# Kernel optimization log

Hardware: AMD Instinct MI355X
Metric: run time of the kernel (lower is better)

## Reference

```python
import jax, jax.numpy as jnp
import numpy as np

D_MODEL = 1024
EXPAND = 2
HEADDIM = 64
D_STATE = 64
CHUNK = 64
D_INNER = EXPAND * D_MODEL          # 2048
NHEADS = D_INNER // HEADDIM         # 32
D_MLP = int(2.5 * D_MODEL)          # 2560
BATCH = 2
SEQLEN = 4096
PROJ = 2 * D_INNER + 2 * NHEADS * D_STATE + NHEADS + NHEADS * (D_STATE // 2)


def rmsnorm(x, w, eps=1e-5):
    return x * jax.lax.rsqrt(jnp.mean(x * x, axis=-1, keepdims=True) + eps) * w


def apply_rope(x, angles):
    x1 = x[..., 0::2]
    x2 = x[..., 1::2]
    c = jnp.cos(angles)
    s = jnp.sin(angles)
    ev = c * x1 - s * x2
    od = s * x1 + c * x2
    return jnp.stack([ev, od], axis=-1).reshape(x.shape)


def segsum(x):
    # x: (b,h,c,l) -> (b,h,c,l,l); [i,j] = sum_{j<k<=i} x_k (no -inf mask, as in source)
    T = x.shape[-1]
    xx = jnp.broadcast_to(x[..., :, None], x.shape + (T,))
    mask = jnp.tril(jnp.ones((T, T), dtype=bool), -1)
    xx = jnp.where(mask, xx, 0.0)
    return jnp.cumsum(xx, axis=-2)


def ssd(x, A, B, C, chunk):
    # x: (b,s,h,p), A: (b,s,h), B/C: (b,s,h,n); s % chunk == 0
    b, s, h, p = x.shape
    n = B.shape[-1]
    c = s // chunk
    x_c = x.reshape(b, c, chunk, h, p).transpose(0, 1, 3, 2, 4)  # (b,c,h,l,p)
    B_c = B.reshape(b, c, chunk, h, n).transpose(0, 1, 3, 2, 4)  # (b,c,h,l,n)
    C_c = C.reshape(b, c, chunk, h, n).transpose(0, 1, 3, 2, 4)
    A_c = A.reshape(b, c, chunk, h).transpose(0, 1, 3, 2)        # (b,c,h,l)
    A_cum = jnp.cumsum(A_c, axis=-1)
    L = jnp.exp(segsum(A_c.transpose(0, 2, 1, 3))).transpose(0, 2, 1, 3, 4)  # (b,c,h,l,l)
    Bx = jnp.einsum('bchln,bchlp->bchpn', B_c, x_c)
    Y_diag = jnp.einsum('bchln,bchls,bchpn->bchlp', C_c, L, Bx)
    decay_states = jnp.exp(A_cum[..., -1:] - A_cum)
    states = jnp.einsum('bchln,bchl,bchlp->bchpn', B_c, decay_states, x_c)  # (b,c,h,p,n)
    decay_chunk = jnp.exp(A_cum[..., -1])  # (b,c,h)
    h0 = jnp.zeros_like(states[:, 0])

    def step(carry, inp):
        dec, st = inp  # dec: (b,h), st: (b,h,p,n)
        carry = carry * dec[:, :, None, None] + st
        return carry, carry

    _, hs = jax.lax.scan(step, h0, (decay_chunk.transpose(1, 0, 2),
                                    states.transpose(1, 0, 2, 3, 4)))
    final_states = hs.transpose(1, 0, 2, 3, 4)  # (b,c,h,p,n)
    Y_off = jnp.einsum('bchln,bchpn,bchl->bchlp', C_c, final_states, jnp.exp(A_cum))
    Y = (Y_diag + Y_off).transpose(0, 1, 3, 2, 4).reshape(b, s, h * p)
    return Y


def setup_inputs() -> dict:
    key = jax.random.key(0)
    ks = jax.random.split(key, 12)
    sc = 0.02
    return {
        'x': jax.random.normal(ks[0], (BATCH, SEQLEN, D_MODEL), jnp.float32),
        'norm1_w': jnp.ones((D_MODEL,), jnp.float32),
        'norm2_w': jnp.ones((D_MODEL,), jnp.float32),
        'W_in': sc * jax.random.normal(ks[1], (D_MODEL, PROJ), jnp.float32),
        'W_out': sc * jax.random.normal(ks[2], (D_INNER, D_MODEL), jnp.float32),
        'A_log': jax.random.uniform(ks[3], (NHEADS,), jnp.float32, -4.0, -1.0),
        'D_param': jnp.ones((NHEADS,), jnp.float32),
        'dt_bias': jax.random.uniform(ks[4], (NHEADS,), jnp.float32, 0.001, 0.1),
        'B_bias': jnp.ones((1, NHEADS, D_STATE), jnp.float32),
        'C_bias': jnp.ones((1, NHEADS, D_STATE), jnp.float32),
        'Bn_w': jnp.ones((D_STATE,), jnp.float32),
        'Cn_w': jnp.ones((D_STATE,), jnp.float32),
        'Wg': sc * jax.random.normal(ks[5], (D_MODEL, D_MLP), jnp.float32),
        'Wu': sc * jax.random.normal(ks[6], (D_MODEL, D_MLP), jnp.float32),
        'Wd': sc * jax.random.normal(ks[7], (D_MLP, D_MODEL), jnp.float32),
    }


def reference(x, norm1_w, norm2_w, W_in, W_out, A_log, D_param, dt_bias,
              B_bias, C_bias, Bn_w, Cn_w, Wg, Wu, Wd):
    b, s, _ = x.shape
    h = rmsnorm(x, norm1_w)
    proj = h @ W_in
    i = 0
    z = proj[..., i:i + D_INNER]; i += D_INNER
    x_ssm = proj[..., i:i + D_INNER]; i += D_INNER
    B = proj[..., i:i + NHEADS * D_STATE].reshape(b, s, NHEADS, D_STATE); i += NHEADS * D_STATE
    C = proj[..., i:i + NHEADS * D_STATE].reshape(b, s, NHEADS, D_STATE); i += NHEADS * D_STATE
    dt = proj[..., i:i + NHEADS]; i += NHEADS
    theta = proj[..., i:].reshape(b, s, NHEADS, D_STATE // 2)
    dt = jax.nn.softplus(dt + dt_bias)                 # (b,s,h)
    A = -jnp.exp(A_log) * dt
    alpha = jnp.exp(A)
    gamma = (alpha - 1.0) / (A + 1e-6) * 0.5 + 1.0
    B = rmsnorm(B, Bn_w) + B_bias
    C = rmsnorm(C, Cn_w) + C_bias
    cum_theta = jnp.cumsum(dt[..., None] * theta, axis=1)
    B = apply_rope(B, cum_theta)
    C = apply_rope(C, cum_theta)
    x_ssm = x_ssm.reshape(b, s, NHEADS, HEADDIM)
    y = ssd(x_ssm * gamma[..., None], A, B, C, CHUNK)
    skip = jnp.broadcast_to((D_param * x_ssm.sum(-1))[..., None], x_ssm.shape)
    y = y + skip.reshape(b, s, -1)
    y = y * (z * jax.nn.sigmoid(z))
    y = y @ W_out
    x = x + y
    h2 = rmsnorm(x, norm2_w)
    g = h2 @ Wg
    x = x + ((g * jax.nn.sigmoid(g)) * (h2 @ Wu)) @ Wd
    return x
```

## Files before the change

### kernel.cpp

```cpp
#include <hip/hip_runtime.h>
#include <cstdint>
#include <cmath>


typedef __bf16 bf16;
typedef __bf16 bf16x2 __attribute__((ext_vector_type(2)));
typedef __bf16 bf16x4 __attribute__((ext_vector_type(4)));
typedef __bf16 bf16x8 __attribute__((ext_vector_type(8)));
typedef float fx4 __attribute__((ext_vector_type(4)));

#define DEV __device__ __forceinline__

#define OFF_PROJ    0ull
#define OFF_HHI     134217728ull
#define OFF_HLO     150994944ull
#define OFF_WTIN    167772160ull
#define OFF_WTHI    184549376ull
#define OFF_WTLO    186908672ull
#define OFF_PROJT   189267968ull
#define OFF_BX      189267968ull
#define OFF_STATES  222822400ull
#define OFF_WTOUT   222822400ull
#define OFF_WTGU    227016704ull
#define OFF_WTD     237502464ull
#define OFF_ABUF    256376832ull
#define OFF_XSUM    257425408ull
#define OFF_ROWSUM  258473984ull
#define OFF_EXPA    260571136ull
#define OFF_DCHUNK  262668288ull
#define OFF_GAMMA   262684672ull
#define WS_NEEDED   263733248ull

#define OFF_GU      0ull
#define OFF_MBF     83886080ull

DEV void async_copy16(void* lds, const void* gptr) {
  __builtin_amdgcn_global_load_lds(
      (const __attribute__((address_space(1))) unsigned int*)(gptr),
      (__attribute__((address_space(3))) unsigned int*)(lds),
      16, 0, 0);
}

DEV float warp_sum64(float v) {
  #pragma unroll
  for (int o = 32; o; o >>= 1) v += __shfl_xor(v, o);
  return v;
}

DEV float red16(float v) {
  v += __shfl_xor(v, 1); v += __shfl_xor(v, 2);
  v += __shfl_xor(v, 4); v += __shfl_xor(v, 8);
  return v;
}

DEV float softplus_f(float x) { return x > 20.f ? x : log1pf(expf(x)); }
DEV float sigmoid_f(float x) { return 1.f / (1.f + expf(-x)); }

__global__ __launch_bounds__(256) void transpose_cast(
    const float* __restrict__ src, int ld, int col0,
    bf16* __restrict__ dst, int R, int C)
{
  __shared__ float tile[32][33];
  const int c0 = blockIdx.x * 32, r0 = blockIdx.y * 32;
  const int tx = threadIdx.x & 31, ty = threadIdx.x >> 5;
  #pragma unroll
  for (int ii = 0; ii < 4; ++ii) {
    int i = ty + ii * 8;
    int c = c0 + tx;
    tile[i][tx] = (c < C) ? src[(size_t)(r0 + i) * ld + col0 + c] : 0.f;
  }
  __syncthreads();
  #pragma unroll
  for (int ii = 0; ii < 4; ++ii) {
    int i = ty + ii * 8;
    dst[(size_t)(c0 + i) * R + r0 + tx] = (bf16)tile[tx][i];
  }
}

__global__ __launch_bounds__(256) void transpose_cast_hilo(
    const float* __restrict__ src, int ld, int col0,
    bf16* __restrict__ dhi, bf16* __restrict__ dlo, int R, int C)
{
  __shared__ float tile[32][33];
  const int c0 = blockIdx.x * 32, r0 = blockIdx.y * 32;
  const int tx = threadIdx.x & 31, ty = threadIdx.x >> 5;
  #pragma unroll
  for (int ii = 0; ii < 4; ++ii) {
    int i = ty + ii * 8;
    int c = c0 + tx;
    tile[i][tx] = (c < C) ? src[(size_t)(r0 + i) * ld + col0 + c] : 0.f;
  }
  __syncthreads();
  #pragma unroll
  for (int ii = 0; ii < 4; ++ii) {
    int i = ty + ii * 8;
    float v = tile[tx][i];
    bf16 hi = (bf16)v;
    size_t o = (size_t)(c0 + i) * R + r0 + tx;
    dhi[o] = hi;
    dlo[o] = (bf16)(v - (float)hi);
  }
}

__global__ __launch_bounds__(256) void rmsnorm_kernel(
    const float* __restrict__ x, const float* __restrict__ w,
    bf16* __restrict__ hi, bf16* __restrict__ lo)
{
  __shared__ float red[4];
  const size_t row = blockIdx.x;
  const int tid = threadIdx.x;
  float4 v = ((const float4*)(x + row * 1024))[tid];
  float ss = v.x * v.x + v.y * v.y + v.z * v.z + v.w * v.w;
  ss = warp_sum64(ss);
  if ((tid & 63) == 0) red[tid >> 6] = ss;
  __syncthreads();
  float tot = red[0] + red[1] + red[2] + red[3];
  float s = rsqrtf(tot * (1.f / 1024.f) + 1e-5f);
  float4 wv = ((const float4*)w)[tid];
  float h0 = v.x * s * wv.x, h1 = v.y * s * wv.y, h2 = v.z * s * wv.z, h3 = v.w * s * wv.w;
  bf16x4 hv = { (bf16)h0, (bf16)h1, (bf16)h2, (bf16)h3 };
  *(bf16x4*)(hi + row * 1024 + tid * 4) = hv;
  if (lo) {
    bf16x4 lv = { (bf16)(h0 - (float)hv[0]), (bf16)(h1 - (float)hv[1]),
                  (bf16)(h2 - (float)hv[2]), (bf16)(h3 - (float)hv[3]) };
    *(bf16x4*)(lo + row * 1024 + tid * 4) = lv;
  }
}

template <int MODE>
__global__ __launch_bounds__(256) void gemm_bt(
    const bf16* A, const bf16* B, void* Cout, const float* resid,
    int K, int lda, int ldc)
{
  __shared__ bf16 As[128 * 64];
  __shared__ bf16 Bs[128 * 64];
  const int tid = threadIdx.x, wid = tid >> 6, lane = tid & 63;
  const int m0 = blockIdx.y * 128, n0 = blockIdx.x * 128;
  const int wm = (wid & 1) * 64, wn = (wid >> 1) * 64;
  fx4 acc[4][4];
  #pragma unroll
  for (int i = 0; i < 4; ++i)
    #pragma unroll
    for (int j = 0; j < 4; ++j) { fx4 z = {0.f, 0.f, 0.f, 0.f}; acc[i][j] = z; }

  const int srow = wid * 32 + (lane >> 3);
  const int slot = lane & 7;

  for (int k0 = 0; k0 < K; k0 += 64) {
    __syncthreads();
    #pragma unroll
    for (int i = 0; i < 4; ++i) {
      int m = srow + i * 8;
      int cA = ((slot ^ (m & 7)) * 8);
      async_copy16(&As[wid * 2048 + i * 512], A + (size_t)(m0 + m) * lda + k0 + cA);
    }
    #pragma unroll
    for (int i = 0; i < 4; ++i) {
      int n = srow + i * 8;
      int cB = ((slot ^ (n & 7)) * 8);
      async_copy16(&Bs[wid * 2048 + i * 512], B + (size_t)(n0 + n) * K + k0 + cB);
    }
    __syncthreads();
    #pragma unroll
    for (int kk = 0; kk < 2; ++kk) {
      bf16x8 af[4], bfr[4];
      #pragma unroll
      for (int i = 0; i < 4; ++i) {
        int mm = wm + i * 16 + (lane & 15);
        int sA = (kk * 4 + (lane >> 4)) ^ (mm & 7);
        af[i] = *(const bf16x8*)&As[mm * 64 + sA * 8];
        int nn = wn + i * 16 + (lane & 15);
        int sB = (kk * 4 + (lane >> 4)) ^ (nn & 7);
        bfr[i] = *(const bf16x8*)&Bs[nn * 64 + sB * 8];
      }
      #pragma unroll
      for (int i = 0; i < 4; ++i)
        #pragma unroll
        for (int j = 0; j < 4; ++j)
          acc[i][j] = __builtin_amdgcn_mfma_f32_16x16x32_bf16(af[i], bfr[j], acc[i][j], 0, 0, 0);
    }
  }
  const int r0 = (lane >> 4) * 4, cc = lane & 15;
  #pragma unroll
  for (int i = 0; i < 4; ++i) {
    #pragma unroll
    for (int j = 0; j < 4; ++j) {
      #pragma unroll
      for (int r = 0; r < 4; ++r) {
        int m = m0 + wm + i * 16 + r0 + r;
        int n = n0 + wn + j * 16 + cc;
        size_t off = (size_t)m * ldc + n;
        float v = acc[i][j][r];
        if (MODE == 1) ((bf16*)Cout)[off] = (bf16)v;
        else ((float*)Cout)[off] = v + resid[off];
      }
    }
  }
}

__global__ __launch_bounds__(256) void gemm_tail(
    const bf16* Ahi, const bf16* Alo, const bf16* Whi, const bf16* Wlo,
    float* Cout)
{
  __shared__ bf16 Ah[128 * 64], Al[128 * 64], Bh[128 * 64], Bl[128 * 64];
  const int tid = threadIdx.x, wid = tid >> 6, lane = tid & 63;
  const int m0 = blockIdx.y * 128, n0 = blockIdx.x * 128;
  const int wm = (wid & 1) * 64, wn = (wid >> 1) * 64;
  fx4 acc[4][4];
  #pragma unroll
  for (int i = 0; i < 4; ++i)
    #pragma unroll
    for (int j = 0; j < 4; ++j) { fx4 z = {0.f, 0.f, 0.f, 0.f}; acc[i][j] = z; }

  const int srow = wid * 32 + (lane >> 3);
  const int slot = lane & 7;

  for (int k0 = 0; k0 < 1024; k0 += 64) {
    __syncthreads();
    #pragma unroll
    for (int i = 0; i < 4; ++i) {
      int m = srow + i * 8;
      int cA = ((slot ^ (m & 7)) * 8);
      size_t ao = (size_t)(m0 + m) * 1024 + k0 + cA;
      async_copy16(&Ah[wid * 2048 + i * 512], Ahi + ao);
      async_copy16(&Al[wid * 2048 + i * 512], Alo + ao);
      int n = srow + i * 8;
      int cB = ((slot ^ (n & 7)) * 8);
      size_t bo = (size_t)(n0 + n) * 1024 + k0 + cB;
      async_copy16(&Bh[wid * 2048 + i * 512], Whi + bo);
      async_copy16(&Bl[wid * 2048 + i * 512], Wlo + bo);
    }
    __syncthreads();
    #pragma unroll
    for (int kk = 0; kk < 2; ++kk) {
      bf16x8 ah[4], al[4], bh[4], bl[4];
      #pragma unroll
      for (int i = 0; i < 4; ++i) {
        int mm = wm + i * 16 + (lane & 15);
        int sA = (kk * 4 + (lane >> 4)) ^ (mm & 7);
        ah[i] = *(const bf16x8*)&Ah[mm * 64 + sA * 8];
        al[i] = *(const bf16x8*)&Al[mm * 64 + sA * 8];
        int nn = wn + i * 16 + (lane & 15);
        int sB = (kk * 4 + (lane >> 4)) ^ (nn & 7);
        bh[i] = *(const bf16x8*)&Bh[nn * 64 + sB * 8];
        bl[i] = *(const bf16x8*)&Bl[nn * 64 + sB * 8];
      }
      #pragma unroll
      for (int i = 0; i < 4; ++i)
        #pragma unroll
        for (int j = 0; j < 4; ++j) {
          acc[i][j] = __builtin_amdgcn_mfma_f32_16x16x32_bf16(ah[i], bh[j], acc[i][j], 0, 0, 0);
          acc[i][j] = __builtin_amdgcn_mfma_f32_16x16x32_bf16(ah[i], bl[j], acc[i][j], 0, 0, 0);
          acc[i][j] = __builtin_amdgcn_mfma_f32_16x16x32_bf16(al[i], bh[j], acc[i][j], 0, 0, 0);
        }
    }
  }
  const int r0 = (lane >> 4) * 4, cc = lane & 15;
  #pragma unroll
  for (int i = 0; i < 4; ++i)
    #pragma unroll
    for (int j = 0; j < 4; ++j)
      #pragma unroll
      for (int r = 0; r < 4; ++r) {
        int m = m0 + wm + i * 16 + r0 + r;
        int n = n0 + wn + j * 16 + cc;
        Cout[(size_t)m * 1152 + n] = acc[i][j][r];
      }
}

__global__ __launch_bounds__(256) void dt_kernel(
    float* projT, const float* __restrict__ A_log, const float* __restrict__ dt_bias,
    float* __restrict__ a_buf, float* __restrict__ gamma_buf)
{
  const int idx = blockIdx.x * 256 + threadIdx.x;
  const int t = idx >> 5, h = idx & 31;
  float dtr = projT[(size_t)t * 1152 + h] + dt_bias[h];
  float dt = softplus_f(dtr);
  float a = -expf(A_log[h]) * dt;
  float alpha = expf(a);
  float gamma = (alpha - 1.f) / (a + 1e-6f) * 0.5f + 1.f;
  projT[(size_t)t * 1152 + h] = dt;
  a_buf[idx] = a;
  gamma_buf[idx] = gamma;
}

__global__ __launch_bounds__(512, 2) void gemm_proj256(
    const bf16* __restrict__ A, const bf16* __restrict__ B, bf16* __restrict__ Cout,
    const float* __restrict__ gamma_buf, float* __restrict__ xsum,
    const float* __restrict__ Bn_w, const float* __restrict__ Cn_w,
    const float* __restrict__ B_bias, const float* __restrict__ C_bias)
{
  __shared__ bf16 lds[65536];
  const int tid = threadIdx.x, wid = tid >> 6, lane = tid & 63;
  const int bid = blockIdx.x;
  const int swz = (bid & 7) * 128 + (bid >> 3);
  const int by = swz >> 5, bx = swz & 31;
  const int m0 = by * 256, n0 = bx * 256;
  const int wr = wid >> 2, wc = wid & 3;
  const int fl = lane & 15, fq = lane >> 4;
  const int rloc = wid * 8 + (lane >> 3);
  const int colSwz = ((lane & 7) ^ (lane >> 3)) * 8;

  fx4 acc[8][4];
  #pragma unroll
  for (int i = 0; i < 8; ++i)
    #pragma unroll
    for (int j = 0; j < 4; ++j) { fx4 z = {0.f, 0.f, 0.f, 0.f}; acc[i][j] = z; }

  const bf16* gA = A + (size_t)(m0 + rloc) * 1024 + colSwz;
  const bf16* gB = B + (size_t)(n0 + rloc) * 1024 + colSwz;

  auto STAGE = [&](int u, int h) {
    const bf16* s = (h < 2) ? gB : gA;
    s += (size_t)(h & 1) * 128 * 1024 + u * 64;
    bf16* d = &lds[((u & 1) * 4 + h) * 8192 + wid * 512];
    async_copy16(d, s);
    async_copy16(d + 4096, s + 64 * 1024);
  };

  STAGE(0, 0); STAGE(0, 1); STAGE(0, 2); STAGE(0, 3);
  STAGE(1, 0); STAGE(1, 1);
  asm volatile("s_waitcnt vmcnt(4)" ::: "memory");
  __builtin_amdgcn_s_barrier();

  const int NT = 16;
  bf16x8 bfrag[4][2];
  for (int t = 0; t < NT; ++t) {
    const int Bb = (t & 1) * 32768;
    const int Ab = Bb + 16384;
    #pragma unroll
    for (int p = 0; p < 4; ++p) {
      bf16x8 af[2][2];
      if (p == 0) {
        #pragma unroll
        for (int j = 0; j < 4; ++j) {
          int nn = wc * 64 + j * 16 + fl;
          #pragma unroll
          for (int kk = 0; kk < 2; ++kk) {
            int q = (kk * 4 + fq) ^ (nn & 7);
            bfrag[j][kk] = *(const bf16x8*)&lds[Bb + nn * 64 + q * 8];
          }
        }
      }
      #pragma unroll
      for (int ii = 0; ii < 2; ++ii) {
        int mm = wr * 128 + (p * 2 + ii) * 16 + fl;
        #pragma unroll
        for (int kk = 0; kk < 2; ++kk) {
          int q = (kk * 4 + fq) ^ (mm & 7);
          af[ii][kk] = *(const bf16x8*)&lds[Ab + mm * 64 + q * 8];
        }
      }
      {
        int H = 4 * t + 6 + p;
        if (H < 4 * NT) STAGE(H >> 2, H & 3);
      }
      if (p == 3) asm volatile("s_waitcnt vmcnt(4)" ::: "memory");
      __builtin_amdgcn_s_barrier();
      asm volatile("s_waitcnt lgkmcnt(0)" ::: "memory");
      __builtin_amdgcn_sched_barrier(0);
      __builtin_amdgcn_s_setprio(1);
      #pragma unroll
      for (int ii = 0; ii < 2; ++ii)
        #pragma unroll
        for (int j = 0; j < 4; ++j)
          #pragma unroll
          for (int kk = 0; kk < 2; ++kk)
            acc[p * 2 + ii][j] = __builtin_amdgcn_mfma_f32_16x16x32_bf16(
                af[ii][kk], bfrag[j][kk], acc[p * 2 + ii][j], 0, 0, 0);
      __builtin_amdgcn_s_setprio(0);
      __builtin_amdgcn_s_barrier();
    }
  }

  const int reg = bx >> 3;
  const int hh = ((n0 + wc * 64) & 2047) >> 6;
  const int mwb = m0 + wr * 128;
  const int nwb = n0 + wc * 64;
  if (reg == 0) {
    #pragma unroll
    for (int i = 0; i < 8; ++i)
      #pragma unroll
      for (int j = 0; j < 4; ++j)
        #pragma unroll
        for (int r = 0; r < 4; ++r) {
          int m = mwb + i * 16 + fq * 4 + r;
          int n = nwb + j * 16 + fl;
          Cout[(size_t)m * 8192 + n] = (bf16)acc[i][j][r];
        }
  } else if (reg == 1) {
    #pragma unroll
    for (int i = 0; i < 8; ++i)
      #pragma unroll
      for (int r = 0; r < 4; ++r) {
        float s = acc[i][0][r] + acc[i][1][r] + acc[i][2][r] + acc[i][3][r];
        s = red16(s);
        int m = mwb + i * 16 + fq * 4 + r;
        if (fl == 0) xsum[(size_t)m * 32 + hh] = s;
        float g = gamma_buf[(size_t)m * 32 + hh];
        #pragma unroll
        for (int j = 0; j < 4; ++j) {
          int n = nwb + j * 16 + fl;
          Cout[(size_t)m * 8192 + n] = (bf16)(acc[i][j][r] * g);
        }
      }
  } else {
    const float* w = (reg == 2) ? Bn_w : Cn_w;
    const float* bias = (reg == 2) ? B_bias : C_bias;
    #pragma unroll
    for (int i = 0; i < 8; ++i)
      #pragma unroll
      for (int r = 0; r < 4; ++r) {
        float ss = acc[i][0][r] * acc[i][0][r] + acc[i][1][r] * acc[i][1][r]
                 + acc[i][2][r] * acc[i][2][r] + acc[i][3][r] * acc[i][3][r];
        ss = red16(ss);
        float sc = rsqrtf(ss * (1.f / 64.f) + 1e-5f);
        int m = mwb + i * 16 + fq * 4 + r;
        #pragma unroll
        for (int j = 0; j < 4; ++j) {
          int c = j * 16 + fl;
          Cout[(size_t)m * 8192 + nwb + c] =
              (bf16)(acc[i][j][r] * sc * w[c] + bias[hh * 64 + c]);
        }
      }
  }
}

__global__ __launch_bounds__(256) void chunk_sum_kernel(
    const float* __restrict__ projT, float* __restrict__ S)
{
  __shared__ float lds[8 * 288];
  const int blk = blockIdx.x;
  const int hq = blockIdx.y;
  const size_t row0 = (size_t)blk * 64;
  const int tid = threadIdx.x;
  float s = 0.f;
  #pragma unroll 1
  for (int batch = 0; batch < 8; ++batch) {
    __syncthreads();
    const float* src = projT + (row0 + batch * 8) * 1152;
    #pragma unroll
    for (int i = 0; i < 9; ++i) {
      int idx = i * 256 + tid;
      int r = idx / 288, col = idx - r * 288;
      int gcol = (col < 32) ? col : (32 + hq * 256 + (col - 32));
      lds[idx] = src[r * 1152 + gcol];
    }
    __syncthreads();
    int hl = tid >> 5, d = tid & 31;
    #pragma unroll
    for (int r = 0; r < 8; ++r)
      s += lds[r * 288 + hq * 8 + hl] * lds[r * 288 + 32 + hl * 32 + d];
  }
  S[(size_t)blk * 1024 + hq * 256 + tid] = s;
}

__global__ __launch_bounds__(256) void rope_kernel(
    bf16* proj, const float* __restrict__ projT, const float* __restrict__ S)
{
  __shared__ float angs[64 * 33], angc[64 * 33];
  const int blk = blockIdx.x;
  const int b = blk >> 11, c = (blk >> 5) & 63, h = blk & 31;
  const size_t t0 = (size_t)b * 4096 + c * 64;
  const int w = threadIdx.x >> 6, lane = threadIdx.x & 63;
  const float* tr = projT + (t0 + lane) * 1152;
  float dtv = tr[h];
  const float* thp = tr + 32 + h * 32 + w * 8;
  float4 th0 = *(const float4*)thp;
  float4 th1 = *(const float4*)(thp + 4);
  const float* Sp = S + (size_t)(b * 64 + lane) * 1024 + h * 32 + w * 8;
  float4 S0 = *(const float4*)Sp;
  float4 S1 = *(const float4*)(Sp + 4);
  float th[8] = { th0.x, th0.y, th0.z, th0.w, th1.x, th1.y, th1.z, th1.w };
  float Sv[8] = { S0.x, S0.y, S0.z, S0.w, S1.x, S1.y, S1.z, S1.w };
  #pragma unroll 1
  for (int j = 0; j < 8; ++j) {
    int d = w * 8 + j;
    float sv = (lane < c) ? Sv[j] : 0.f;
    float off = warp_sum64(sv);
    float v = dtv * th[j];
    #pragma unroll
    for (int o = 1; o < 64; o <<= 1) { float u = __shfl_up(v, o); if (lane >= o) v += u; }
    float ang = off + v;
    float sn, cs;
    sincosf(ang, &sn, &cs);
    angs[lane * 33 + d] = sn;
    angc[lane * 33 + d] = cs;
  }
  __syncthreads();
  const int tt = threadIdx.x >> 2, q = threadIdx.x & 3;
  const size_t base = (t0 + tt) * 8192 + 4096 + h * 64 + q * 16;
  #pragma unroll
  for (int m = 0; m < 2; ++m) {
    bf16* p = proj + base + m * 2048;
    bf16x8 v0 = *(const bf16x8*)(p);
    bf16x8 v1 = *(const bf16x8*)(p + 8);
    bf16x8 r0, r1;
    #pragma unroll
    for (int pp = 0; pp < 4; ++pp) {
      int d = q * 8 + pp;
      float e1 = (float)v0[2 * pp], e2 = (float)v0[2 * pp + 1];
      float sn = angs[tt * 33 + d], cs = angc[tt * 33 + d];
      r0[2 * pp]     = (bf16)(cs * e1 - sn * e2);
      r0[2 * pp + 1] = (bf16)(sn * e1 + cs * e2);
    }
    #pragma unroll
    for (int pp = 0; pp < 4; ++pp) {
      int d = q * 8 + 4 + pp;
      float e1 = (float)v1[2 * pp], e2 = (float)v1[2 * pp + 1];
      float sn = angs[tt * 33 + d], cs = angc[tt * 33 + d];
      r1[2 * pp]     = (bf16)(cs * e1 - sn * e2);
      r1[2 * pp + 1] = (bf16)(sn * e1 + cs * e2);
    }
    *(bf16x8*)(p) = r0;
    *(bf16x8*)(p + 8) = r1;
  }
}

__global__ __launch_bounds__(256) void ssd1_kernel(
    const bf16* __restrict__ proj, const float* __restrict__ a_buf,
    bf16* __restrict__ Bx, bf16* __restrict__ states,
    float* __restrict__ rowsum, float* __restrict__ expac, float* __restrict__ dchunk)
{
  __shared__ bf16 Xs[64 * 72], Bs[64 * 72];
  __shared__ float acum[64], dsv[64];
  const int blk = blockIdx.x;
  const int h = blk & 31;
  const size_t bs0 = ((size_t)(blk >> 5)) * 64;
  const int tid = threadIdx.x;
  const int l = tid >> 2, p0 = (tid & 3) * 16;
  {
    const bf16* xrow = proj + (bs0 + l) * 8192 + 2048 + h * 64 + p0;
    *(bf16x8*)&Xs[l * 72 + p0]     = ((const bf16x8*)xrow)[0];
    *(bf16x8*)&Xs[l * 72 + p0 + 8] = ((const bf16x8*)xrow)[1];
    const bf16* brow = proj + (bs0 + l) * 8192 + 4096 + h * 64 + p0;
    *(bf16x8*)&Bs[l * 72 + p0]     = ((const bf16x8*)brow)[0];
    *(bf16x8*)&Bs[l * 72 + p0 + 8] = ((const bf16x8*)brow)[1];
  }
  if (tid < 64) {
    float v = a_buf[(bs0 + tid) * 32 + h];
    #pragma unroll
    for (int o = 1; o < 64; o <<= 1) { float u = __shfl_up(v, o); if (tid >= o) v += u; }
    acum[tid] = v;
    float a63 = __shfl(v, 63);
    dsv[tid] = expf(a63 - v);
    expac[(size_t)blk * 64 + tid] = expf(v);
    if (tid == 63) dchunk[blk] = expf(v);
  }
  __syncthreads();
  {
    float al = acum[l];
    float rs = 0.f;
    for (int s = tid & 3; s <= l; s += 4) rs += expf(al - acum[s]);
    rs += __shfl_xor(rs, 1);
    rs += __shfl_xor(rs, 2);
    if ((tid & 3) == 0) rowsum[(size_t)blk * 64 + l] = rs + (float)(63 - l);
  }
  const int wv = tid >> 6, lane = tid & 63;
  const int mi = lane & 15, kq = lane >> 4;
  const int m0 = wv * 16;
  fx4 accB[4], accS[4];
  #pragma unroll
  for (int j4 = 0; j4 < 4; ++j4) { fx4 z = {0.f,0.f,0.f,0.f}; accB[j4] = z; accS[j4] = z; }
  #pragma unroll
  for (int kk = 0; kk < 2; ++kk) {
    const int lb = kk * 32 + kq * 8;
    bf16x8 aX, aXd;
    #pragma unroll
    for (int j = 0; j < 8; ++j) {
      bf16 xv = Xs[(lb + j) * 72 + m0 + mi];
      aX[j] = xv;
      aXd[j] = (bf16)((float)xv * dsv[lb + j]);
    }
    #pragma unroll
    for (int j4 = 0; j4 < 4; ++j4) {
      bf16x8 bB;
      #pragma unroll
      for (int j = 0; j < 8; ++j) bB[j] = Bs[(lb + j) * 72 + j4 * 16 + mi];
      accB[j4] = __builtin_amdgcn_mfma_f32_16x16x32_bf16(aX, bB, accB[j4], 0, 0, 0);
      accS[j4] = __builtin_amdgcn_mfma_f32_16x16x32_bf16(aXd, bB, accS[j4], 0, 0, 0);
    }
  }
  const size_t obase = (size_t)blk * 4096;
  #pragma unroll
  for (int j4 = 0; j4 < 4; ++j4) {
    #pragma unroll
    for (int r = 0; r < 4; ++r) {
      int p = m0 + kq * 4 + r;
      int n = j4 * 16 + mi;
      Bx[obase + p * 64 + n] = (bf16)accB[j4][r];
      states[obase + p * 64 + n] = (bf16)accS[j4][r];
    }
  }
}

__global__ __launch_bounds__(128) void ssd2_kernel(
    bf16* __restrict__ states, const float* __restrict__ dchunk)
{
  const int blk = blockIdx.x;
  const int b = blk >> 9, rest = blk & 511;
  const int h = rest >> 4, q = rest & 15;
  const int e0 = q * 256 + threadIdx.x * 2;
  float fs0 = 0.f, fs1 = 0.f;
  #pragma unroll 2
  for (int c = 0; c < 64; ++c) {
    size_t idx = ((size_t)(b * 2048 + c * 32 + h) * 4096) + e0;
    float dec = dchunk[b * 2048 + c * 32 + h];
    bf16x2 st = *(const bf16x2*)(states + idx);
    fs0 = fs0 * dec + (float)st[0];
    fs1 = fs1 * dec + (float)st[1];
    bf16x2 o = { (bf16)fs0, (bf16)fs1 };
    *(bf16x2*)(states + idx) = o;
  }
}

__global__ __launch_bounds__(256) void ssd3_kernel(
    bf16* proj, const bf16* __restrict__ Bx, const bf16* __restrict__ FS,
    const float* __restrict__ rowsum, const float* __restrict__ expac,
    const float* __restrict__ xsum, const float* __restrict__ D_param)
{
  __shared__ bf16 Cs[64 * 72], BxS[64 * 72], FSs[64 * 72];
  __shared__ float rs_s[64], ea_s[64], sk_s[64];
  const int blk = blockIdx.x;
  const int h = blk & 31;
  const size_t bs0 = ((size_t)(blk >> 5)) * 64;
  const int tid = threadIdx.x;
  const int l = tid >> 2, q0 = (tid & 3) * 16;
  {
    const bf16* crow = proj + (bs0 + l) * 8192 + 6144 + h * 64 + q0;
    *(bf16x8*)&Cs[l * 72 + q0]     = ((const bf16x8*)crow)[0];
    *(bf16x8*)&Cs[l * 72 + q0 + 8] = ((const bf16x8*)crow)[1];
    size_t mb = (size_t)blk * 4096 + l * 64 + q0;
    *(bf16x8*)&BxS[l * 72 + q0]     = ((const bf16x8*)(Bx + mb))[0];
    *(bf16x8*)&BxS[l * 72 + q0 + 8] = ((const bf16x8*)(Bx + mb))[1];
    *(bf16x8*)&FSs[l * 72 + q0]     = ((const bf16x8*)(FS + mb))[0];
    *(bf16x8*)&FSs[l * 72 + q0 + 8] = ((const bf16x8*)(FS + mb))[1];
  }
  if (tid < 64) {
    rs_s[tid] = rowsum[(size_t)blk * 64 + tid];
    ea_s[tid] = expac[(size_t)blk * 64 + tid];
    sk_s[tid] = D_param[h] * xsum[(bs0 + tid) * 32 + h];
  }
  __syncthreads();
  const int wv = tid >> 6, lane = tid & 63;
  const int mi = lane & 15, kq = lane >> 4;
  const int m0 = wv * 16;
  fx4 acc1[4], acc2[4];
  #pragma unroll
  for (int j4 = 0; j4 < 4; ++j4) { fx4 z = {0.f,0.f,0.f,0.f}; acc1[j4] = z; acc2[j4] = z; }
  #pragma unroll
  for (int kk = 0; kk < 2; ++kk) {
    bf16x8 aC = *(const bf16x8*)&Cs[(m0 + mi) * 72 + kk * 32 + kq * 8];
    #pragma unroll
    for (int j4 = 0; j4 < 4; ++j4) {
      bf16x8 bx = *(const bf16x8*)&BxS[(j4 * 16 + mi) * 72 + kk * 32 + kq * 8];
      bf16x8 fs = *(const bf16x8*)&FSs[(j4 * 16 + mi) * 72 + kk * 32 + kq * 8];
      acc1[j4] = __builtin_amdgcn_mfma_f32_16x16x32_bf16(aC, bx, acc1[j4], 0, 0, 0);
      acc2[j4] = __builtin_amdgcn_mfma_f32_16x16x32_bf16(aC, fs, acc2[j4], 0, 0, 0);
    }
  }
  #pragma unroll
  for (int j4 = 0; j4 < 4; ++j4) {
    #pragma unroll
    for (int r = 0; r < 4; ++r) {
      int li = m0 + kq * 4 + r;
      int p = j4 * 16 + mi;
      float y = rs_s[li] * acc1[j4][r] + ea_s[li] * acc2[j4][r] + sk_s[li];
      size_t zoff = (bs0 + li) * 8192 + h * 64 + p;
      float z = (float)proj[zoff];
      proj[zoff + 2048] = (bf16)(y * z * sigmoid_f(z));
    }
  }
}

__global__ __launch_bounds__(256) void silu_mul_kernel(
    const bf16* __restrict__ gu, bf16* __restrict__ m)
{
  const size_t row = blockIdx.y;
  const int col2 = blockIdx.x * 256 + threadIdx.x;
  const size_t gi = row * 5120 + col2 * 2;
  bf16x2 g = *(const bf16x2*)(gu + gi);
  bf16x2 u = *(const bf16x2*)(gu + gi + 2560);
  float g0 = (float)g[0], g1 = (float)g[1];
  float m0 = g0 * sigmoid_f(g0) * (float)u[0];
  float m1 = g1 * sigmoid_f(g1) * (float)u[1];
  bf16x2 mv = { (bf16)m0, (bf16)m1 };
  *(bf16x2*)(m + row * 2560 + col2 * 2) = mv;
}

extern "C" void kernel_launch(void* const* d_in, const int* in_sizes, int n_in,
                              void* d_out, int out_size, void* d_ws, size_t ws_size,
                              hipStream_t stream) {
  (void)in_sizes; (void)n_in; (void)out_size;
  if (ws_size < WS_NEEDED) return;
  const float* x       = (const float*)d_in[0];
  const float* n1w     = (const float*)d_in[1];
  const float* n2w     = (const float*)d_in[2];
  const float* W_in    = (const float*)d_in[3];
  const float* W_out   = (const float*)d_in[4];
  const float* A_log   = (const float*)d_in[5];
  const float* D_param = (const float*)d_in[6];
  const float* dt_bias = (const float*)d_in[7];
  const float* B_bias  = (const float*)d_in[8];
  const float* C_bias  = (const float*)d_in[9];
  const float* Bn_w    = (const float*)d_in[10];
  const float* Cn_w    = (const float*)d_in[11];
  const float* Wg      = (const float*)d_in[12];
  const float* Wu      = (const float*)d_in[13];
  const float* Wd      = (const float*)d_in[14];
  float* out = (float*)d_out;
  char* ws = (char*)d_ws;

  bf16*  proj   = (bf16*)(ws + OFF_PROJ);
  float* projT  = (float*)(ws + OFF_PROJT);
  bf16*  h_hi   = (bf16*)(ws + OFF_HHI);
  bf16*  h_lo   = (bf16*)(ws + OFF_HLO);
  bf16*  Wt_in  = (bf16*)(ws + OFF_WTIN);
  bf16*  Wt_hi  = (bf16*)(ws + OFF_WTHI);
  bf16*  Wt_lo  = (bf16*)(ws + OFF_WTLO);
  bf16*  Wt_out = (bf16*)(ws + OFF_WTOUT);
  bf16*  Wt_gu  = (bf16*)(ws + OFF_WTGU);
  bf16*  Wt_d   = (bf16*)(ws + OFF_WTD);
  bf16*  Bx     = (bf16*)(ws + OFF_BX);
  bf16*  states = (bf16*)(ws + OFF_STATES);
  float* a_buf  = (float*)(ws + OFF_ABUF);
  float* xsum_  = (float*)(ws + OFF_XSUM);
  float* rowsum = (float*)(ws + OFF_ROWSUM);
  float* expac  = (float*)(ws + OFF_EXPA);
  float* dchunk = (float*)(ws + OFF_DCHUNK);
  float* gamma_ = (float*)(ws + OFF_GAMMA);
  float* Ssum   = (float*)(ws + OFF_HLO);
  bf16*  ybf    = proj + 2048;
  bf16*  gubf   = (bf16*)(ws + OFF_GU);
  bf16*  mbf    = (bf16*)(ws + OFF_MBF);
  bf16*  h2bf   = h_hi;
  float* x2     = out;

  transpose_cast<<<dim3(256, 32), 256, 0, stream>>>(W_in, 9248, 0, Wt_in, 1024, 8192);
  transpose_cast_hilo<<<dim3(36, 32), 256, 0, stream>>>(W_in, 9248, 8192, Wt_hi, Wt_lo, 1024, 1056);

  rmsnorm_kernel<<<8192, 256, 0, stream>>>(x, n1w, h_hi, h_lo);

  gemm_tail<<<dim3(9, 64), 256, 0, stream>>>(h_hi, h_lo, Wt_hi, Wt_lo, projT);
  dt_kernel<<<1024, 256, 0, stream>>>(projT, A_log, dt_bias, a_buf, gamma_);
  gemm_proj256<<<dim3(1024), 512, 0, stream>>>(h_hi, Wt_in, proj, gamma_, xsum_,
                                               Bn_w, Cn_w, B_bias, C_bias);

  chunk_sum_kernel<<<dim3(128, 4), 256, 0, stream>>>(projT, Ssum);
  rope_kernel<<<4096, 256, 0, stream>>>(proj, projT, Ssum);

  ssd1_kernel<<<4096, 256, 0, stream>>>(proj, a_buf, Bx, states, rowsum, expac, dchunk);
  ssd2_kernel<<<1024, 128, 0, stream>>>(states, dchunk);
  ssd3_kernel<<<4096, 256, 0, stream>>>(proj, Bx, states, rowsum, expac, xsum_, D_param);

  transpose_cast<<<dim3(32, 64), 256, 0, stream>>>(W_out, 1024, 0, Wt_out, 2048, 1024);
  transpose_cast<<<dim3(80, 32), 256, 0, stream>>>(Wg, 2560, 0, Wt_gu, 1024, 2560);
  transpose_cast<<<dim3(80, 32), 256, 0, stream>>>(Wu, 2560, 0, Wt_gu + (size_t)2560 * 1024, 1024, 2560);
  transpose_cast<<<dim3(32, 80), 256, 0, stream>>>(Wd, 1024, 0, Wt_d, 2560, 1024);

  gemm_bt<2><<<dim3(8, 64), 256, 0, stream>>>(ybf, Wt_out, x2, x, 2048, 8192, 1024);

  rmsnorm_kernel<<<8192, 256, 0, stream>>>(x2, n2w, h2bf, nullptr);
  gemm_bt<1><<<dim3(40, 64), 256, 0, stream>>>(h2bf, Wt_gu, gubf, nullptr, 1024, 1024, 5120);
  silu_mul_kernel<<<dim3(5, 8192), 256, 0, stream>>>(gubf, mbf);
  gemm_bt<2><<<dim3(8, 64), 256, 0, stream>>>(mbf, Wt_d, out, x2, 2560, 2560, 1024);
}
```

Measured before the change: 812.9 us.

## Use 256x256-tile pipelined bf16 GEMM for the MLP gate/up projection

Replaces the generic gemm_bt call for the fused gate/up projection (8192x1024 by 5120) with a new 256x256-tile kernel of 512 threads. It uses double-buffered async global-to-LDS copies, an XOR-swizzled LDS layout, a block-index swizzle for L2 locality, and interleaved MFMA phases with priority hints. The aim is more data reuse per tile and better overlap of loads with compute. The cost is a large LDS footprint and high register use, which limit occupancy, plus a grid of 640 blocks that may leave the tail unbalanced.

```diff
diff --git a/kernel.cpp b/kernel.cpp
--- a/kernel.cpp
+++ b/kernel.cpp
@@ -424,6 +424,109 @@
         }
       }
   }
+}
+
+__global__ __launch_bounds__(512, 2) void gemm256_bf16(
+    const bf16* __restrict__ A, const bf16* __restrict__ B, bf16* __restrict__ Cout,
+    int NT, int lda, int ldc, int nbx)
+{
+  __shared__ bf16 lds[65536];
+  const int tid = threadIdx.x, wid = tid >> 6, lane = tid & 63;
+  const int cpx = gridDim.x >> 3;
+  const int bid = blockIdx.x;
+  const int swz = (bid & 7) * cpx + (bid >> 3);
+  const int by = swz / nbx, bx = swz - by * nbx;
+  const int m0 = by * 256, n0 = bx * 256;
+  const int wr = wid >> 2, wc = wid & 3;
+  const int fl = lane & 15, fq = lane >> 4;
+  const int rloc = wid * 8 + (lane >> 3);
+  const int colSwz = ((lane & 7) ^ (lane >> 3)) * 8;
+  const int K = NT * 64;
+
+  fx4 acc[8][4];
+  #pragma unroll
+  for (int i = 0; i < 8; ++i)
+    #pragma unroll
+    for (int j = 0; j < 4; ++j) { fx4 z = {0.f, 0.f, 0.f, 0.f}; acc[i][j] = z; }
+
+  const bf16* gA = A + (size_t)(m0 + rloc) * lda + colSwz;
+  const bf16* gB = B + (size_t)(n0 + rloc) * K + colSwz;
+
+  auto STAGE = [&](int u, int h) {
+    const bf16* s = (h < 2) ? gB : gA;
+    const size_t str = (h < 2) ? (size_t)K : (size_t)lda;
+    s += (size_t)(h & 1) * 128 * str + u * 64;
+    bf16* d = &lds[((u & 1) * 4 + h) * 8192 + wid * 512];
+    async_copy16(d, s);
+    async_copy16(d + 4096, s + 64 * str);
+  };
+
+  STAGE(0, 0); STAGE(0, 1); STAGE(0, 2); STAGE(0, 3);
+  STAGE(1, 0); STAGE(1, 1);
+  asm volatile("s_waitcnt vmcnt(4)" ::: "memory");
+  __builtin_amdgcn_s_barrier();
+
+  bf16x8 bfrag[4][2];
+  for (int t = 0; t < NT; ++t) {
+    const int Bb = (t & 1) * 32768;
+    const int Ab = Bb + 16384;
+    #pragma unroll
+    for (int p = 0; p < 4; ++p) {
+      bf16x8 af[2][2];
+      if (p == 0) {
+        #pragma unroll
+        for (int j = 0; j < 4; ++j) {
+          int nn = wc * 64 + j * 16 + fl;
+          #pragma unroll
+          for (int kk = 0; kk < 2; ++kk) {
+            int q = (kk * 4 + fq) ^ (nn & 7);
+            bfrag[j][kk] = *(const bf16x8*)&lds[Bb + nn * 64 + q * 8];
+          }
+        }
+      }
+      #pragma unroll
+      for (int ii = 0; ii < 2; ++ii) {
+        int mm = wr * 128 + (p * 2 + ii) * 16 + fl;
+        #pragma unroll
+        for (int kk = 0; kk < 2; ++kk) {
+          int q = (kk * 4 + fq) ^ (mm & 7);
+          af[ii][kk] = *(const bf16x8*)&lds[Ab + mm * 64 + q * 8];
+        }
+      }
+      {
+        int H = 4 * t + 6 + p;
+        if (H < 4 * NT) STAGE(H >> 2, H & 3);
+      }
+      if (p == 3) asm volatile("s_waitcnt vmcnt(4)" ::: "memory");
+      __builtin_amdgcn_s_barrier();
+      asm volatile("s_waitcnt lgkmcnt(0)" ::: "memory");
+      __builtin_amdgcn_sched_barrier(0);
+      __builtin_amdgcn_s_setprio(1);
+      #pragma unroll
+      for (int ii = 0; ii < 2; ++ii)
+        #pragma unroll
+        for (int j = 0; j < 4; ++j)
+          #pragma unroll
+          for (int kk = 0; kk < 2; ++kk)
+            acc[p * 2 + ii][j] = __builtin_amdgcn_mfma_f32_16x16x32_bf16(
+                af[ii][kk], bfrag[j][kk], acc[p * 2 + ii][j], 0, 0, 0);
+      __builtin_amdgcn_s_setprio(0);
+      __builtin_amdgcn_s_barrier();
+    }
+  }
+
+  const int mwb = m0 + wr * 128;
+  const int nwb = n0 + wc * 64;
+  #pragma unroll
+  for (int i = 0; i < 8; ++i)
+    #pragma unroll
+    for (int j = 0; j < 4; ++j)
+      #pragma unroll
+      for (int r = 0; r < 4; ++r) {
+        int m = mwb + i * 16 + fq * 4 + r;
+        int n = nwb + j * 16 + fl;
+        Cout[(size_t)m * ldc + n] = (bf16)acc[i][j][r];
+      }
 }
 
 __global__ __launch_bounds__(256) void chunk_sum_kernel(
@@ -761,7 +864,7 @@
   gemm_bt<2><<<dim3(8, 64), 256, 0, stream>>>(ybf, Wt_out, x2, x, 2048, 8192, 1024);
 
   rmsnorm_kernel<<<8192, 256, 0, stream>>>(x2, n2w, h2bf, nullptr);
-  gemm_bt<1><<<dim3(40, 64), 256, 0, stream>>>(h2bf, Wt_gu, gubf, nullptr, 1024, 1024, 5120);
+  gemm256_bf16<<<dim3(640), 512, 0, stream>>>(h2bf, Wt_gu, gubf, 16, 1024, 5120, 20);
   silu_mul_kernel<<<dim3(5, 8192), 256, 0, stream>>>(gubf, mbf);
   gemm_bt<2><<<dim3(8, 64), 256, 0, stream>>>(mbf, Wt_d, out, x2, 2560, 2560, 1024);
 }
```

New measurement: 831.7 us. 2.3% more time.

## Replace output and MLP GEMMs with pipelined 128x256 double-buffered kernel

Applied to the files above, without the earlier changes.

Replaces the simple 128x128 single-stage GEMM used for the out-projection and MLP with a 512-thread 128x256 tile kernel. It double-buffers LDS with staggered async copies interleaved among the MFMA phases, uses grouped block-index swizzling for L2 locality, and raises wave priority around MFMA bursts. The goal is to hide global-load latency and raise MFMA utilisation. In exchange it uses more LDS (96KB per block) and more barriers, and it assumes dimensions divide the tile sizes.

```diff
diff --git a/kernel.cpp b/kernel.cpp
--- a/kernel.cpp
+++ b/kernel.cpp
@@ -127,77 +127,6 @@
   }
 }
 
-template <int MODE>
-__global__ __launch_bounds__(256) void gemm_bt(
-    const bf16* A, const bf16* B, void* Cout, const float* resid,
-    int K, int lda, int ldc)
-{
-  __shared__ bf16 As[128 * 64];
-  __shared__ bf16 Bs[128 * 64];
-  const int tid = threadIdx.x, wid = tid >> 6, lane = tid & 63;
-  const int m0 = blockIdx.y * 128, n0 = blockIdx.x * 128;
-  const int wm = (wid & 1) * 64, wn = (wid >> 1) * 64;
-  fx4 acc[4][4];
-  #pragma unroll
-  for (int i = 0; i < 4; ++i)
-    #pragma unroll
-    for (int j = 0; j < 4; ++j) { fx4 z = {0.f, 0.f, 0.f, 0.f}; acc[i][j] = z; }
-
-  const int srow = wid * 32 + (lane >> 3);
-  const int slot = lane & 7;
-
-  for (int k0 = 0; k0 < K; k0 += 64) {
-    __syncthreads();
-    #pragma unroll
-    for (int i = 0; i < 4; ++i) {
-      int m = srow + i * 8;
-      int cA = ((slot ^ (m & 7)) * 8);
-      async_copy16(&As[wid * 2048 + i * 512], A + (size_t)(m0 + m) * lda + k0 + cA);
-    }
-    #pragma unroll
-    for (int i = 0; i < 4; ++i) {
-      int n = srow + i * 8;
-      int cB = ((slot ^ (n & 7)) * 8);
-      async_copy16(&Bs[wid * 2048 + i * 512], B + (size_t)(n0 + n) * K + k0 + cB);
-    }
-    __syncthreads();
-    #pragma unroll
-    for (int kk = 0; kk < 2; ++kk) {
-      bf16x8 af[4], bfr[4];
-      #pragma unroll
-      for (int i = 0; i < 4; ++i) {
-        int mm = wm + i * 16 + (lane & 15);
-        int sA = (kk * 4 + (lane >> 4)) ^ (mm & 7);
-        af[i] = *(const bf16x8*)&As[mm * 64 + sA * 8];
-        int nn = wn + i * 16 + (lane & 15);
-        int sB = (kk * 4 + (lane >> 4)) ^ (nn & 7);
-        bfr[i] = *(const bf16x8*)&Bs[nn * 64 + sB * 8];
-      }
-      #pragma unroll
-      for (int i = 0; i < 4; ++i)
-        #pragma unroll
-        for (int j = 0; j < 4; ++j)
-          acc[i][j] = __builtin_amdgcn_mfma_f32_16x16x32_bf16(af[i], bfr[j], acc[i][j], 0, 0, 0);
-    }
-  }
-  const int r0 = (lane >> 4) * 4, cc = lane & 15;
-  #pragma unroll
-  for (int i = 0; i < 4; ++i) {
-    #pragma unroll
-    for (int j = 0; j < 4; ++j) {
-      #pragma unroll
-      for (int r = 0; r < 4; ++r) {
-        int m = m0 + wm + i * 16 + r0 + r;
-        int n = n0 + wn + j * 16 + cc;
-        size_t off = (size_t)m * ldc + n;
-        float v = acc[i][j][r];
-        if (MODE == 1) ((bf16*)Cout)[off] = (bf16)v;
-        else ((float*)Cout)[off] = v + resid[off];
-      }
-    }
-  }
-}
-
 __global__ __launch_bounds__(256) void gemm_tail(
     const bf16* Ahi, const bf16* Alo, const bf16* Whi, const bf16* Wlo,
     float* Cout)
@@ -424,6 +353,110 @@
         }
       }
   }
+}
+
+template <int MODE>
+__global__ __launch_bounds__(512, 2) void gemm128x256(
+    const bf16* __restrict__ A, const bf16* __restrict__ B, void* __restrict__ Cout,
+    const float* __restrict__ resid, int NT, int lda, int ldc, int nbx)
+{
+  __shared__ bf16 lds[49152];
+  const int tid = threadIdx.x, wid = tid >> 6, lane = tid & 63;
+  const int cpx = gridDim.x >> 3;
+  const int bid = blockIdx.x;
+  const int swz = (bid & 7) * cpx + (bid >> 3);
+  const int by = swz / nbx, bx = swz - by * nbx;
+  const int m0 = by * 128, n0 = bx * 256;
+  const int wr = wid >> 2, wc = wid & 3;
+  const int fl = lane & 15, fq = lane >> 4;
+  const int rloc = wid * 8 + (lane >> 3);
+  const int colSwz = ((lane & 7) ^ (lane >> 3)) * 8;
+  const int K = NT * 64;
+
+  fx4 acc[4][4];
+  #pragma unroll
+  for (int i = 0; i < 4; ++i)
+    #pragma unroll
+    for (int j = 0; j < 4; ++j) { fx4 z = {0.f, 0.f, 0.f, 0.f}; acc[i][j] = z; }
+
+  const bf16* gA = A + (size_t)(m0 + rloc) * lda + colSwz;
+  const bf16* gB = B + (size_t)(n0 + rloc) * K + colSwz;
+
+  auto STAGE = [&](int u, int h) {
+    const bf16* s;
+    size_t str;
+    if (h < 2) { s = gB + (size_t)h * 128 * K; str = (size_t)K; }
+    else       { s = gA;                       str = (size_t)lda; }
+    s += u * 64;
+    bf16* d = &lds[((u & 1) * 3 + h) * 8192 + wid * 512];
+    async_copy16(d, s);
+    async_copy16(d + 4096, s + 64 * str);
+  };
+
+  STAGE(0, 0); STAGE(0, 1); STAGE(0, 2);
+  STAGE(1, 0); STAGE(1, 1);
+  asm volatile("s_waitcnt vmcnt(4)" ::: "memory");
+  __builtin_amdgcn_s_barrier();
+
+  bf16x8 bfrag[4][2];
+  for (int t = 0; t < NT; ++t) {
+    const int base = (t & 1) * 24576;
+    #pragma unroll
+    for (int p = 0; p < 4; ++p) {
+      bf16x8 af[2];
+      if (p == 0) {
+        #pragma unroll
+        for (int j = 0; j < 4; ++j) {
+          int nn = wc * 64 + j * 16 + fl;
+          #pragma unroll
+          for (int kk = 0; kk < 2; ++kk) {
+            int q = (kk * 4 + fq) ^ (nn & 7);
+            bfrag[j][kk] = *(const bf16x8*)&lds[base + (nn >> 7) * 8192 + (nn & 127) * 64 + q * 8];
+          }
+        }
+      }
+      {
+        int mm = wr * 64 + p * 16 + fl;
+        #pragma unroll
+        for (int kk = 0; kk < 2; ++kk) {
+          int q = (kk * 4 + fq) ^ (mm & 7);
+          af[kk] = *(const bf16x8*)&lds[base + 2 * 8192 + mm * 64 + q * 8];
+        }
+      }
+      if (p == 0)      { if (t + 1 < NT) STAGE(t + 1, 2); }
+      else if (p == 1) { if (t + 2 < NT) STAGE(t + 2, 0); }
+      else if (p == 2) { if (t + 2 < NT) STAGE(t + 2, 1); }
+      if (p == 3) asm volatile("s_waitcnt vmcnt(4)" ::: "memory");
+      __builtin_amdgcn_s_barrier();
+      asm volatile("s_waitcnt lgkmcnt(0)" ::: "memory");
+      __builtin_amdgcn_sched_barrier(0);
+      __builtin_amdgcn_s_setprio(1);
+      #pragma unroll
+      for (int j = 0; j < 4; ++j)
+        #pragma unroll
+        for (int kk = 0; kk < 2; ++kk)
+          acc[p][j] = __builtin_amdgcn_mfma_f32_16x16x32_bf16(
+              af[kk], bfrag[j][kk], acc[p][j], 0, 0, 0);
+      __builtin_amdgcn_s_setprio(0);
+      __builtin_amdgcn_s_barrier();
+    }
+  }
+
+  const int mwb = m0 + wr * 64;
+  const int nwb = n0 + wc * 64;
+  #pragma unroll
+  for (int i = 0; i < 4; ++i)
+    #pragma unroll
+    for (int j = 0; j < 4; ++j)
+      #pragma unroll
+      for (int r = 0; r < 4; ++r) {
+        int m = mwb + i * 16 + fq * 4 + r;
+        int n = nwb + j * 16 + fl;
+        size_t off = (size_t)m * ldc + n;
+        float v = acc[i][j][r];
+        if (MODE == 1) ((bf16*)Cout)[off] = (bf16)v;
+        else ((float*)Cout)[off] = v + resid[off];
+      }
 }
 
 __global__ __launch_bounds__(256) void chunk_sum_kernel(
@@ -758,10 +791,10 @@
   transpose_cast<<<dim3(80, 32), 256, 0, stream>>>(Wu, 2560, 0, Wt_gu + (size_t)2560 * 1024, 1024, 2560);
   transpose_cast<<<dim3(32, 80), 256, 0, stream>>>(Wd, 1024, 0, Wt_d, 2560, 1024);
 
-  gemm_bt<2><<<dim3(8, 64), 256, 0, stream>>>(ybf, Wt_out, x2, x, 2048, 8192, 1024);
+  gemm128x256<2><<<dim3(256), 512, 0, stream>>>(ybf, Wt_out, x2, x, 32, 8192, 1024, 4);
 
   rmsnorm_kernel<<<8192, 256, 0, stream>>>(x2, n2w, h2bf, nullptr);
-  gemm_bt<1><<<dim3(40, 64), 256, 0, stream>>>(h2bf, Wt_gu, gubf, nullptr, 1024, 1024, 5120);
+  gemm128x256<1><<<dim3(1280), 512, 0, stream>>>(h2bf, Wt_gu, gubf, nullptr, 16, 1024, 5120, 20);
   silu_mul_kernel<<<dim3(5, 8192), 256, 0, stream>>>(gubf, mbf);
-  gemm_bt<2><<<dim3(8, 64), 256, 0, stream>>>(mbf, Wt_d, out, x2, 2560, 2560, 1024);
-}
+  gemm128x256<2><<<dim3(256), 512, 0, stream>>>(mbf, Wt_d, out, x2, 40, 2560, 1024, 4);
+}
```

Result: faster. 783.0 us (-3.7%).
